# Performance work log

Measured on AMD Instinct MI355X. Metric: run time of the kernel, lower is better.

The kernel has to match this reference:

```python
import jax, jax.numpy as jnp
import numpy as np

NBINS = 256
HMIN, HMAX = 0.0, 255.0

def _histc(x, nbins=NBINS, lo=HMIN, hi=HMAX):
    # Faithful torch.histc: bin width (hi-lo)/nbins; values outside [lo,hi] ignored;
    # values == hi fall into the last bin. Returns float counts.
    xf = x.reshape(-1)
    width = (hi - lo) / nbins
    idx = jnp.floor((xf - lo) / width).astype(jnp.int32)
    idx = jnp.minimum(idx, nbins - 1)            # x == hi -> last bin
    in_range = (xf >= lo) & (xf <= hi)
    idx = jnp.where(in_range, idx, nbins)        # out-of-range -> dropped bucket
    hist = jnp.zeros(nbins + 1, dtype=x.dtype).at[idx].add(1.0)
    return hist[:nbins]

def setup_inputs() -> dict:
    key = jax.random.key(0)
    # intensity image with values in [0, 255]
    x = jax.random.uniform(key, (8192, 4096), dtype=jnp.float32) * 255.0
    return {"batchsize": 16, "input": x}

def reference(batchsize, input):
    hist = _histc(input)                          # [256] float counts
    # Original loop recomputes the same histc each iter and does
    # count += hist[0] (scalar broadcast into all 256 slots).
    count = jnp.zeros(NBINS, dtype=hist.dtype) + jnp.asarray(batchsize, hist.dtype) * hist[0]
    return (hist, count)
```

## Files before the change

### kernel.cpp

```cpp
#include <hip/hip_runtime.h>

#define NBINS 256
#define NWAVES 4
#define BLOCK 256
#define GRID 2048

#define BIN_SCALE (256.0f / 255.0f)

__global__ void zero_out(float* __restrict__ out) {
    const int i = blockIdx.x * blockDim.x + threadIdx.x;
    if (i < 2 * NBINS) out[i] = 0.0f;
}

__device__ __forceinline__ void bin_one(float v, unsigned int* sh_wave) {
    if (v >= 0.0f && v <= 255.0f) {
        int idx = (int)(v * BIN_SCALE);
        atomicAdd(&sh_wave[min(idx, NBINS - 1)], 1u);
    }
}

__global__ __launch_bounds__(BLOCK) void hist_kernel(const float* __restrict__ x,
                                                     float* __restrict__ out,
                                                     int n) {
    __shared__ unsigned int sh[NWAVES][NBINS];
    unsigned int* sh_wave = sh[threadIdx.x >> 6];

    for (int i = threadIdx.x; i < NWAVES * NBINS; i += BLOCK)
        ((unsigned int*)sh)[i] = 0u;
    __syncthreads();

    const int n4 = n >> 2;
    const float4* __restrict__ x4 = (const float4*)x;
    const int tid = blockIdx.x * BLOCK + threadIdx.x;
    const int stride = gridDim.x * BLOCK;

    for (int i = tid; i < n4; i += stride) {
        float4 v = x4[i];
        bin_one(v.x, sh_wave);
        bin_one(v.y, sh_wave);
        bin_one(v.z, sh_wave);
        bin_one(v.w, sh_wave);
    }

    for (int i = (n4 << 2) + tid; i < n; i += stride)
        bin_one(x[i], sh_wave);

    __syncthreads();

    for (int b = threadIdx.x; b < NBINS; b += BLOCK) {
        unsigned int s = sh[0][b] + sh[1][b] + sh[2][b] + sh[3][b];
        if (s) atomicAdd(&out[b], (float)s);
    }
}

__global__ void count_kernel(const void* __restrict__ bs_raw,
                             float* __restrict__ out) {
    const int as_int = *(const int*)bs_raw;
    float bs;
    if (as_int >= 1 && as_int < (1 << 20)) {
        bs = (float)as_int;
    } else {
        bs = *(const float*)bs_raw;
    }
    out[NBINS + threadIdx.x] = bs * out[0];
}

extern "C" void kernel_launch(void* const* d_in, const int* in_sizes, int n_in,
                              void* d_out, int out_size, void* d_ws, size_t ws_size,
                              hipStream_t stream) {
    const void* bs_ptr;
    const float* x;
    int n;
    if (n_in >= 2 && in_sizes[0] == 1) {
        bs_ptr = d_in[0];
        x = (const float*)d_in[1];
        n = in_sizes[1];
    } else {
        bs_ptr = d_in[1];
        x = (const float*)d_in[0];
        n = in_sizes[0];
    }

    float* out = (float*)d_out;

    zero_out<<<2, 256, 0, stream>>>(out);
    hist_kernel<<<GRID, BLOCK, 0, stream>>>(x, out, n);
    count_kernel<<<1, NBINS, 0, stream>>>(bs_ptr, out);
}
```

Measured before the change: 230.8 us.

## Use per-thread byte-counter histograms in LDS instead of per-wave atomics

Each thread gets a private 256-entry byte histogram in LDS, 64KB per block, so bins are incremented without shared-memory atomics. The private histograms are then reduced across threads with packed 4-byte reads before the global float atomics. The grid is sized so each thread handles at most 200 elements, which keeps the byte counters from overflowing. The large LDS footprint limits occupancy, and byte read-modify-writes can hit bank conflicts.

New measurement: 276.2 us. +19.7%, slower.

```diff
diff --git a/kernel.cpp b/kernel.cpp
--- a/kernel.cpp
+++ b/kernel.cpp
@@ -1,10 +1,7 @@
 #include <hip/hip_runtime.h>
 
 #define NBINS 256
-#define NWAVES 4
 #define BLOCK 256
-#define GRID 2048
-
 #define BIN_SCALE (256.0f / 255.0f)
 
 __global__ void zero_out(float* __restrict__ out) {
@@ -12,22 +9,17 @@
     if (i < 2 * NBINS) out[i] = 0.0f;
 }
 
-__device__ __forceinline__ void bin_one(float v, unsigned int* sh_wave) {
-    if (v >= 0.0f && v <= 255.0f) {
-        int idx = (int)(v * BIN_SCALE);
-        atomicAdd(&sh_wave[min(idx, NBINS - 1)], 1u);
-    }
-}
-
 __global__ __launch_bounds__(BLOCK) void hist_kernel(const float* __restrict__ x,
                                                      float* __restrict__ out,
                                                      int n) {
-    __shared__ unsigned int sh[NWAVES][NBINS];
-    unsigned int* sh_wave = sh[threadIdx.x >> 6];
+    __shared__ unsigned char priv[BLOCK * NBINS];
+    __shared__ uint4 part[4][64];
 
-    for (int i = threadIdx.x; i < NWAVES * NBINS; i += BLOCK)
-        ((unsigned int*)sh)[i] = 0u;
-    __syncthreads();
+    unsigned char* __restrict__ mine = &priv[threadIdx.x * NBINS];
+
+    uint4* mz = (uint4*)mine;
+#pragma unroll
+    for (int i = 0; i < NBINS / 16; ++i) mz[i] = make_uint4(0u, 0u, 0u, 0u);
 
     const int n4 = n >> 2;
     const float4* __restrict__ x4 = (const float4*)x;
@@ -36,20 +28,39 @@
 
     for (int i = tid; i < n4; i += stride) {
         float4 v = x4[i];
-        bin_one(v.x, sh_wave);
-        bin_one(v.y, sh_wave);
-        bin_one(v.z, sh_wave);
-        bin_one(v.w, sh_wave);
+        if (v.x >= 0.0f && v.x <= 255.0f) mine[min((int)(v.x * BIN_SCALE), NBINS - 1)]++;
+        if (v.y >= 0.0f && v.y <= 255.0f) mine[min((int)(v.y * BIN_SCALE), NBINS - 1)]++;
+        if (v.z >= 0.0f && v.z <= 255.0f) mine[min((int)(v.z * BIN_SCALE), NBINS - 1)]++;
+        if (v.w >= 0.0f && v.w <= 255.0f) mine[min((int)(v.w * BIN_SCALE), NBINS - 1)]++;
     }
-
-    for (int i = (n4 << 2) + tid; i < n; i += stride)
-        bin_one(x[i], sh_wave);
+    for (int i = (n4 << 2) + tid; i < n; i += stride) {
+        float v = x[i];
+        if (v >= 0.0f && v <= 255.0f) mine[min((int)(v * BIN_SCALE), NBINS - 1)]++;
+    }
 
     __syncthreads();
 
-    for (int b = threadIdx.x; b < NBINS; b += BLOCK) {
-        unsigned int s = sh[0][b] + sh[1][b] + sh[2][b] + sh[3][b];
-        if (s) atomicAdd(&out[b], (float)s);
+    const int lane = threadIdx.x & 63;
+    const int w = threadIdx.x >> 6;
+    const unsigned* pw = (const unsigned*)priv;
+    unsigned s0 = 0, s1 = 0, s2 = 0, s3 = 0;
+#pragma unroll 8
+    for (int t = w * 64; t < w * 64 + 64; ++t) {
+        unsigned u = pw[t * 64 + lane];
+        s0 += u & 0xFFu;
+        s1 += (u >> 8) & 0xFFu;
+        s2 += (u >> 16) & 0xFFu;
+        s3 += u >> 24;
+    }
+    part[w][lane] = make_uint4(s0, s1, s2, s3);
+    __syncthreads();
+
+    if (w == 0) {
+        uint4 a = part[0][lane], b = part[1][lane], c = part[2][lane], d = part[3][lane];
+        atomicAdd(&out[lane * 4 + 0], (float)(a.x + b.x + c.x + d.x));
+        atomicAdd(&out[lane * 4 + 1], (float)(a.y + b.y + c.y + d.y));
+        atomicAdd(&out[lane * 4 + 2], (float)(a.z + b.z + c.z + d.z));
+        atomicAdd(&out[lane * 4 + 3], (float)(a.w + b.w + c.w + d.w));
     }
 }
 
@@ -83,7 +94,12 @@
 
     float* out = (float*)d_out;
 
+    int grid = 1024;
+    long threads = (long)grid * BLOCK;
+    long per = ((long)n + threads - 1) / threads;
+    if (per > 200) grid = (int)(((long)n + (long)BLOCK * 200 - 1) / ((long)BLOCK * 200));
+
     zero_out<<<2, 256, 0, stream>>>(out);
-    hist_kernel<<<GRID, BLOCK, 0, stream>>>(x, out, n);
+    hist_kernel<<<grid, BLOCK, 0, stream>>>(x, out, n);
     count_kernel<<<1, NBINS, 0, stream>>>(bs_ptr, out);
 }
```

## Replicate shared histogram 32 ways with bin-major interleaved layout

Applied to the files above, without the earlier changes.

Replaces the four per-wave shared histograms with 32 copies laid out bin-major, so each lane updates its own copy (lane & 31) in a distinct bank. This is meant to remove atomic contention and LDS bank conflicts when many lanes hit the same bin. The final reduction sums the 32 copies per bin with a rotated index to avoid bank conflicts. LDS use grows to 32 KB per block, which may lower occupancy.

New measurement: 220.0 us. -4.6%, faster.

```diff
diff --git a/kernel.cpp b/kernel.cpp
--- a/kernel.cpp
+++ b/kernel.cpp
@@ -1,10 +1,9 @@
 #include <hip/hip_runtime.h>
 
 #define NBINS 256
-#define NWAVES 4
 #define BLOCK 256
 #define GRID 2048
-
+#define NCOPY 32
 #define BIN_SCALE (256.0f / 255.0f)
 
 __global__ void zero_out(float* __restrict__ out) {
@@ -12,21 +11,18 @@
     if (i < 2 * NBINS) out[i] = 0.0f;
 }
 
-__device__ __forceinline__ void bin_one(float v, unsigned int* sh_wave) {
-    if (v >= 0.0f && v <= 255.0f) {
-        int idx = (int)(v * BIN_SCALE);
-        atomicAdd(&sh_wave[min(idx, NBINS - 1)], 1u);
-    }
-}
-
 __global__ __launch_bounds__(BLOCK) void hist_kernel(const float* __restrict__ x,
                                                      float* __restrict__ out,
                                                      int n) {
-    __shared__ unsigned int sh[NWAVES][NBINS];
-    unsigned int* sh_wave = sh[threadIdx.x >> 6];
+    __shared__ unsigned int sh[NBINS * NCOPY];
 
-    for (int i = threadIdx.x; i < NWAVES * NBINS; i += BLOCK)
-        ((unsigned int*)sh)[i] = 0u;
+    const int c = threadIdx.x & 31;
+
+    {
+        uint4* z = (uint4*)&sh[threadIdx.x * 32];
+#pragma unroll
+        for (int i = 0; i < 8; ++i) z[i] = make_uint4(0u, 0u, 0u, 0u);
+    }
     __syncthreads();
 
     const int n4 = n >> 2;
@@ -36,21 +32,30 @@
 
     for (int i = tid; i < n4; i += stride) {
         float4 v = x4[i];
-        bin_one(v.x, sh_wave);
-        bin_one(v.y, sh_wave);
-        bin_one(v.z, sh_wave);
-        bin_one(v.w, sh_wave);
+        if (v.x >= 0.0f && v.x <= 255.0f)
+            atomicAdd(&sh[min((int)(v.x * BIN_SCALE), NBINS - 1) * NCOPY + c], 1u);
+        if (v.y >= 0.0f && v.y <= 255.0f)
+            atomicAdd(&sh[min((int)(v.y * BIN_SCALE), NBINS - 1) * NCOPY + c], 1u);
+        if (v.z >= 0.0f && v.z <= 255.0f)
+            atomicAdd(&sh[min((int)(v.z * BIN_SCALE), NBINS - 1) * NCOPY + c], 1u);
+        if (v.w >= 0.0f && v.w <= 255.0f)
+            atomicAdd(&sh[min((int)(v.w * BIN_SCALE), NBINS - 1) * NCOPY + c], 1u);
     }
-
-    for (int i = (n4 << 2) + tid; i < n; i += stride)
-        bin_one(x[i], sh_wave);
+    for (int i = (n4 << 2) + tid; i < n; i += stride) {
+        float v = x[i];
+        if (v >= 0.0f && v <= 255.0f)
+            atomicAdd(&sh[min((int)(v * BIN_SCALE), NBINS - 1) * NCOPY + c], 1u);
+    }
 
     __syncthreads();
 
-    for (int b = threadIdx.x; b < NBINS; b += BLOCK) {
-        unsigned int s = sh[0][b] + sh[1][b] + sh[2][b] + sh[3][b];
-        if (s) atomicAdd(&out[b], (float)s);
-    }
+    const int b = threadIdx.x;
+    unsigned int s = 0;
+#pragma unroll
+    for (int i = 0; i < NCOPY; ++i)
+        s += sh[b * NCOPY + ((i + b) & 31)];
+
+    if (s) atomicAdd(&out[b], (float)s);
 }
 
 __global__ void count_kernel(const void* __restrict__ bs_raw,
```

## Replace LDS atomics with per-thread packed byte counters and two-stage reduction

Applied to the files above, without the earlier changes.

Each thread now owns a private column of 64 dwords in LDS and packs four 8-bit bin counters into each dword, so binning uses plain read-modify-write instead of shared-memory atomics, with explicit handling when two of the four values hit the same dword. Per-thread work is capped (62 float4 per thread, at most 248 hits per byte) so the 8-bit counters cannot overflow, and the grid is sized from that cap instead of fixed. Per-block partial histograms go to workspace and a separate reduce kernel sums them, removing most global float atomics. The cost is a much larger grid, an extra kernel launch, workspace traffic, and a transposed per-block reduction over 64 dwords per thread.

New measurement: 216.6 us. -6.1%, faster.

```diff
diff --git a/kernel.cpp b/kernel.cpp
--- a/kernel.cpp
+++ b/kernel.cpp
@@ -1,56 +1,104 @@
 #include <hip/hip_runtime.h>
 
 #define NBINS 256
-#define NWAVES 4
-#define BLOCK 256
-#define GRID 2048
-
+#define BLOCK 64
+#define NQUAD 64
+#define CNT_DW (NQUAD * 64)
+#define LDS_DW (CNT_DW + 64)
 #define BIN_SCALE (256.0f / 255.0f)
+#define CAP_F4 62
 
 __global__ void zero_out(float* __restrict__ out) {
     const int i = blockIdx.x * blockDim.x + threadIdx.x;
     if (i < 2 * NBINS) out[i] = 0.0f;
 }
 
-__device__ __forceinline__ void bin_one(float v, unsigned int* sh_wave) {
-    if (v >= 0.0f && v <= 255.0f) {
-        int idx = (int)(v * BIN_SCALE);
-        atomicAdd(&sh_wave[min(idx, NBINS - 1)], 1u);
-    }
+__device__ __forceinline__ void classify(float v, int t, int& dw, unsigned& inc) {
+    int idx = (int)(v * BIN_SCALE);
+    idx = idx < 255 ? idx : 255;
+    const bool ok = (v >= 0.0f) && (v <= 255.0f);
+    const int d = ((((unsigned)idx) >> 2) << 6) + t;
+    dw = ok ? d : (CNT_DW + t);
+    inc = 1u << ((idx & 3) << 3);
 }
 
 __global__ __launch_bounds__(BLOCK) void hist_kernel(const float* __restrict__ x,
+                                                     unsigned int* __restrict__ partial,
                                                      float* __restrict__ out,
-                                                     int n) {
-    __shared__ unsigned int sh[NWAVES][NBINS];
-    unsigned int* sh_wave = sh[threadIdx.x >> 6];
+                                                     int n, int G, int use_ws) {
+    __shared__ unsigned int cnt[LDS_DW];
+    const int t = threadIdx.x;
 
-    for (int i = threadIdx.x; i < NWAVES * NBINS; i += BLOCK)
-        ((unsigned int*)sh)[i] = 0u;
+    for (int i = t; i < LDS_DW; i += BLOCK) cnt[i] = 0u;
     __syncthreads();
 
     const int n4 = n >> 2;
     const float4* __restrict__ x4 = (const float4*)x;
-    const int tid = blockIdx.x * BLOCK + threadIdx.x;
-    const int stride = gridDim.x * BLOCK;
+    const int stride = G * BLOCK;
+    int i = blockIdx.x * BLOCK + t;
 
-    for (int i = tid; i < n4; i += stride) {
+    if (i < n4) {
         float4 v = x4[i];
-        bin_one(v.x, sh_wave);
-        bin_one(v.y, sh_wave);
-        bin_one(v.z, sh_wave);
-        bin_one(v.w, sh_wave);
+        for (;;) {
+            const int ni = i + stride;
+            const bool more = ni < n4;
+            float4 nv;
+            if (more) nv = x4[ni];
+
+            int d0, d1, d2, d3; unsigned s0, s1, s2, s3;
+            classify(v.x, t, d0, s0);
+            classify(v.y, t, d1, s1);
+            classify(v.z, t, d2, s2);
+            classify(v.w, t, d3, s3);
+
+            unsigned o0 = cnt[d0], o1 = cnt[d1], o2 = cnt[d2], o3 = cnt[d3];
+            cnt[d0] = o0 + s0;
+            cnt[d1] = o1 + s1 + (d1 == d0 ? s0 : 0u);
+            cnt[d2] = o2 + s2 + (d2 == d0 ? s0 : 0u) + (d2 == d1 ? s1 : 0u);
+            cnt[d3] = o3 + s3 + (d3 == d0 ? s0 : 0u) + (d3 == d1 ? s1 : 0u)
+                              + (d3 == d2 ? s2 : 0u);
+
+            if (!more) break;
+            v = nv; i = ni;
+        }
     }
-
-    for (int i = (n4 << 2) + tid; i < n; i += stride)
-        bin_one(x[i], sh_wave);
-
+    for (int j = (n4 << 2) + blockIdx.x * BLOCK + t; j < n; j += stride) {
+        int dw; unsigned inc;
+        classify(x[j], t, dw, inc);
+        cnt[dw] += inc;
+    }
     __syncthreads();
 
-    for (int b = threadIdx.x; b < NBINS; b += BLOCK) {
-        unsigned int s = sh[0][b] + sh[1][b] + sh[2][b] + sh[3][b];
-        if (s) atomicAdd(&out[b], (float)s);
+    unsigned accA = 0, accB = 0;
+#pragma unroll 16
+    for (int k = 0; k < 64; ++k) {
+        unsigned u = cnt[(t << 6) + ((t + k) & 63)];
+        accA += u & 0x00FF00FFu;
+        accB += (u >> 8) & 0x00FF00FFu;
     }
+    const unsigned b0 = accA & 0xFFFFu, b2 = accA >> 16;
+    const unsigned b1 = accB & 0xFFFFu, b3 = accB >> 16;
+
+    if (use_ws) {
+        ((uint4*)(partial + (size_t)blockIdx.x * NBINS))[t] = make_uint4(b0, b1, b2, b3);
+    } else {
+        if (b0) atomicAdd(&out[4 * t + 0], (float)b0);
+        if (b1) atomicAdd(&out[4 * t + 1], (float)b1);
+        if (b2) atomicAdd(&out[4 * t + 2], (float)b2);
+        if (b3) atomicAdd(&out[4 * t + 3], (float)b3);
+    }
+}
+
+__global__ __launch_bounds__(NBINS) void reduce_kernel(const unsigned int* __restrict__ partial,
+                                                       float* __restrict__ out,
+                                                       int G, int slice) {
+    const int bin = threadIdx.x;
+    const int g0 = blockIdx.x * slice;
+    const int g1 = (g0 + slice < G) ? (g0 + slice) : G;
+    unsigned s = 0;
+    for (int g = g0; g < g1; ++g)
+        s += partial[(size_t)g * NBINS + bin];
+    if (s) atomicAdd(&out[bin], (float)s);
 }
 
 __global__ void count_kernel(const void* __restrict__ bs_raw,
@@ -82,8 +130,20 @@
     }
 
     float* out = (float*)d_out;
+    unsigned int* partial = (unsigned int*)d_ws;
+
+    const long n4 = (long)n >> 2;
+    int G = (int)((n4 + (long)BLOCK * CAP_F4 - 1) / ((long)BLOCK * CAP_F4));
+    if (G < 1) G = 1;
+
+    const size_t ws_need = (size_t)G * NBINS * sizeof(unsigned int);
+    const int use_ws = (ws_size >= ws_need) ? 1 : 0;
 
     zero_out<<<2, 256, 0, stream>>>(out);
-    hist_kernel<<<GRID, BLOCK, 0, stream>>>(x, out, n);
+    hist_kernel<<<G, BLOCK, 0, stream>>>(x, partial, out, n, G, use_ws);
+    if (use_ws) {
+        const int slice = (G + NBINS - 1) / NBINS;
+        reduce_kernel<<<NBINS, NBINS, 0, stream>>>(partial, out, G, slice);
+    }
     count_kernel<<<1, NBINS, 0, stream>>>(bs_ptr, out);
 }
```
